# Kernel tuning notes

Measured on AMD Instinct MI355X. Metric: run time of the kernel, lower is better.

The kernel has to match this reference:

```python
import jax, jax.numpy as jnp
import numpy as np

NEG_BIG = 1e8  # diagonal mask penalty from the original code


def setup_inputs() -> dict:
    key = jax.random.key(0)
    ks = jax.random.split(key, 8)
    B, N, E, H, D, Hm = 2, 1024, 256, 64, 64, 128
    return {
        "encoder_output": jax.random.normal(ks[0], (B, N, E), dtype=jnp.float32),
        "wl": jax.random.normal(ks[1], (E, H), dtype=jnp.float32) * (1.0 / np.sqrt(E)),
        "wr": jax.random.normal(ks[2], (E, H), dtype=jnp.float32) * (1.0 / np.sqrt(E)),
        "u": jax.random.normal(ks[3], (H,), dtype=jnp.float32) * (1.0 / np.sqrt(H)),
        "l_bias": jnp.zeros((1,), dtype=jnp.float32),
        "edge_query": jax.random.normal(ks[4], (N, D), dtype=jnp.float32),
        "mlp_w1": jax.random.normal(ks[5], (D, Hm), dtype=jnp.float32) * (1.0 / np.sqrt(D)),
        "mlp_b1": jnp.zeros((Hm,), dtype=jnp.float32),
        "mlp_w2": jax.random.normal(ks[6], (Hm, 1), dtype=jnp.float32) * (1.0 / np.sqrt(Hm)),
        "mlp_b2": jnp.zeros((1,), dtype=jnp.float32),
    }


def reference(encoder_output, wl, wr, u, l_bias, edge_query, mlp_w1, mlp_b1, mlp_w2, mlp_b2):
    # edge-weight MLP: [E_edges, d] -> [E_edges]
    w_logits = (jax.nn.relu(edge_query @ mlp_w1 + mlp_b1) @ mlp_w2 + mlp_b2)[:, 0]
    w = jax.nn.softplus(w_logits) + 1e-8

    # pairwise additive attention logits
    dot_l = jnp.einsum("bne,eh->bnh", encoder_output, wl)  # [B,N,H]
    dot_r = jnp.einsum("bne,eh->bnh", encoder_output, wr)  # [B,N,H]
    final_sum = jnp.tanh(dot_l[:, :, None, :] + dot_r[:, None, :, :])  # [B,N,N,H]
    logits = jnp.einsum("bijh,h->bij", final_sum, u) + l_bias[0]  # [B,N,N]

    # vectorized diagonal masking (replaces the per-node python loop)
    N = logits.shape[1]
    eye = jnp.eye(N, dtype=logits.dtype)
    mask_scores = logits - NEG_BIG * eye[None, :, :]  # [B,N,N]

    probs = jax.nn.sigmoid(mask_scores)
    samples = (jax.random.uniform(jax.random.key(1), mask_scores.shape) < probs).astype(logits.dtype)
    # Bernoulli entropy from logits: softplus(l) - l * sigmoid(l)
    entropy = jax.nn.softplus(mask_scores) - mask_scores * probs
    return samples, mask_scores, entropy, w
```

## Files before the change

### kernel.cpp

```cpp
#include <hip/hip_runtime.h>
#include <hip/hip_bf16.h>


#define L2E 1.4426950408889634f
#define C2  2.8853900817779268f
#define LN2 0.6931471805599453f
#define RCP(x) __builtin_amdgcn_rcpf(x)
#define EXP2(x) __builtin_amdgcn_exp2f(x)
#define LOG2(x) __builtin_amdgcn_logf(x)

__device__ __forceinline__ void threefry2x32_01(unsigned x0, unsigned x1,
                                                unsigned& o0, unsigned& o1) {
  const unsigned k0 = 0u, k1 = 1u;
  const unsigned k2 = 0x1BD11BDAu ^ k0 ^ k1;
#define TF_R(r) { x0 += x1; x1 = (x1 << r) | (x1 >> (32 - r)); x1 ^= x0; }
  x0 += k0; x1 += k1;
  TF_R(13) TF_R(15) TF_R(26) TF_R(6)
  x0 += k1; x1 += k2 + 1u;
  TF_R(17) TF_R(29) TF_R(16) TF_R(24)
  x0 += k2; x1 += k0 + 2u;
  TF_R(13) TF_R(15) TF_R(26) TF_R(6)
  x0 += k0; x1 += k1 + 3u;
  TF_R(17) TF_R(29) TF_R(16) TF_R(24)
  x0 += k1; x1 += k2 + 4u;
  TF_R(13) TF_R(15) TF_R(26) TF_R(6)
  x0 += k2; x1 += k0 + 5u;
#undef TF_R
  o0 = x0; o1 = x1;
}

__device__ __forceinline__ float tf_uniform(unsigned y) {
  return __uint_as_float((y >> 9) | 0x3f800000u) - 1.0f;
}

__global__ __launch_bounds__(128) void edge_mlp_kernel(
    const float* __restrict__ eq, const float* __restrict__ w1,
    const float* __restrict__ b1, const float* __restrict__ w2,
    const float* __restrict__ b2, float* __restrict__ wout) {
  __shared__ float eql[64];
  __shared__ float part[2];
  const int t = threadIdx.x;
  const int e = blockIdx.x;
  if (t < 64) eql[t] = eq[e * 64 + t];
  __syncthreads();
  float acc = b1[t];
#pragma unroll 8
  for (int k = 0; k < 64; ++k) acc = fmaf(eql[k], w1[k * 128 + t], acc);
  float v = fmaxf(acc, 0.0f) * w2[t];
#pragma unroll
  for (int off = 32; off > 0; off >>= 1) v += __shfl_down(v, off);
  if ((t & 63) == 0) part[t >> 6] = v;
  __syncthreads();
  if (t == 0) {
    const float l = part[0] + part[1] + b2[0];
    const float sp = fmaxf(l, 0.0f) + log1pf(expf(-fabsf(l)));
    wout[e] = sp + 1e-8f;
  }
}

__global__ __launch_bounds__(256) void proj_exp_kernel(
    const float* __restrict__ enc, const float* __restrict__ wl,
    const float* __restrict__ wr, float* __restrict__ ws) {
  __shared__ float As[32][33];
  __shared__ float Ws[32][34];
  const int t = threadIdx.x;
  const int r0 = blockIdx.x * 32;
  const int c0 = blockIdx.y * 32;
  const float* __restrict__ wmat = (c0 < 64) ? wl : wr;
  const int cbase = c0 & 63;
  const int ty = t >> 4, tx = t & 15;
  float acc[2][2] = {};
  for (int ec = 0; ec < 8; ++ec) {
    {
      const int rr = t >> 3, e4 = (t & 7) * 4;
      const float4 v = *(const float4*)(enc + (r0 + rr) * 256 + ec * 32 + e4);
      As[rr][e4] = v.x; As[rr][e4 + 1] = v.y; As[rr][e4 + 2] = v.z; As[rr][e4 + 3] = v.w;
      const float4 w = *(const float4*)(wmat + (ec * 32 + rr) * 64 + cbase + e4);
      Ws[rr][e4] = w.x; Ws[rr][e4 + 1] = w.y; Ws[rr][e4 + 2] = w.z; Ws[rr][e4 + 3] = w.w;
    }
    __syncthreads();
#pragma unroll
    for (int e = 0; e < 32; ++e) {
      const float a0 = As[2 * ty][e];
      const float a1 = As[2 * ty + 1][e];
      const float2 wv = *(const float2*)&Ws[e][2 * tx];
      acc[0][0] = fmaf(a0, wv.x, acc[0][0]);
      acc[0][1] = fmaf(a0, wv.y, acc[0][1]);
      acc[1][0] = fmaf(a1, wv.x, acc[1][0]);
      acc[1][1] = fmaf(a1, wv.y, acc[1][1]);
    }
    __syncthreads();
  }
  const int matoff = (c0 < 64) ? 0 : 131072;
#pragma unroll
  for (int i = 0; i < 2; ++i) {
    const int r = r0 + 2 * ty + i;
    const int b = r >> 10, n = r & 1023;
#pragma unroll
    for (int j = 0; j < 2; ++j) {
      const int c = cbase + 2 * tx + j;
      ws[matoff + b * 65536 + c * 1024 + n] = EXP2(C2 * acc[i][j]);
    }
  }
}

__global__ __launch_bounds__(256) void pair_kernel(
    const float* __restrict__ ws, const float* __restrict__ u,
    const float* __restrict__ lb, float* __restrict__ out) {
  __shared__ float sA[2 * 64 * 64];
  __shared__ float sB[2 * 64 * 32];
  __shared__ float sU[64];
  const int t = threadIdx.x;
  const int i0 = blockIdx.x * 64;
  const int j0 = blockIdx.y * 32;

#pragma unroll
  for (int b = 0; b < 2; ++b) {
    const float* __restrict__ src = ws + b * 65536;
#pragma unroll
    for (int q = 0; q < 4; ++q) {
      const int h = (t >> 4) + 16 * q;
      const int c = (t & 15) * 4;
      *(float4*)(sA + b * 4096 + h * 64 + c) =
          *(const float4*)(src + h * 1024 + i0 + c);
    }
  }
#pragma unroll
  for (int b = 0; b < 2; ++b) {
    const float* __restrict__ src = ws + 131072 + b * 65536;
#pragma unroll
    for (int q = 0; q < 2; ++q) {
      const int h = (t >> 3) + 32 * q;
      const int c = (t & 7) * 4;
      *(float4*)(sB + b * 2048 + h * 32 + c) =
          *(const float4*)(src + h * 1024 + j0 + c);
    }
  }
  if (t < 64) sU[t] = u[t];
  __syncthreads();

  const int ia = (t >> 4) * 4;
  const int ja = (t & 15) * 2;
  float acc[2][4][2] = {};
#pragma unroll 4
  for (int h = 0; h < 64; ++h) {
    const float uh = sU[h];
#pragma unroll
    for (int b = 0; b < 2; ++b) {
      const float4 av = *(const float4*)(sA + b * 4096 + h * 64 + ia);
      const float2 bv = *(const float2*)(sB + b * 2048 + h * 32 + ja);
      const float a[4] = {av.x, av.y, av.z, av.w};
#pragma unroll
      for (int ii = 0; ii < 4; ++ii) {
        acc[b][ii][0] += uh * RCP(fmaf(a[ii], bv.x, 1.0f));
        acc[b][ii][1] += uh * RCP(fmaf(a[ii], bv.y, 1.0f));
      }
    }
  }

  float uv = sU[t & 63];
#pragma unroll
  for (int off = 32; off > 0; off >>= 1) uv += __shfl_xor(uv, off);
  const float su = uv + lb[0];

  float* __restrict__ outS = out;
  float* __restrict__ outM = out + 2097152;
  float* __restrict__ outE = out + 4194304;
#pragma unroll
  for (int ii = 0; ii < 4; ++ii) {
    const int gi = i0 + ia + ii;
    const unsigned mb = (unsigned)(gi * 1024 + j0 + ja);
    unsigned y00, y01, y10, y11;
    threefry2x32_01(mb, mb + 1048576u, y00, y01);
    threefry2x32_01(mb + 1u, mb + 1u + 1048576u, y10, y11);
    const float uu[2][2] = {{tf_uniform(y00), tf_uniform(y01)},
                            {tf_uniform(y10), tf_uniform(y11)}};
#pragma unroll
    for (int b = 0; b < 2; ++b) {
      float2 sv, ev, smv;
#pragma unroll
      for (int jj = 0; jj < 2; ++jj) {
        const int gj = j0 + ja + jj;
        float s = fmaf(-2.0f, acc[b][ii][jj], su);
        if (gi == gj) s -= 1e8f;
        const float ex = EXP2(-s * L2E);
        const float p = RCP(1.0f + ex);
        const float em = EXP2(-fabsf(s) * L2E);
        const float ent = fmaxf(s, 0.0f) + LOG2(1.0f + em) * LN2 - s * p;
        const float smp = (uu[jj][b] < p) ? 1.0f : 0.0f;
        (&sv.x)[jj] = s;
        (&ev.x)[jj] = ent;
        (&smv.x)[jj] = smp;
      }
      const int base = b * 1048576 + gi * 1024 + (j0 + ja);
      *(float2*)(outS + base) = smv;
      *(float2*)(outM + base) = sv;
      *(float2*)(outE + base) = ev;
    }
  }
}

extern "C" void kernel_launch(void* const* d_in, const int* in_sizes, int n_in,
                              void* d_out, int out_size, void* d_ws, size_t ws_size,
                              hipStream_t stream) {
  const float* enc = (const float*)d_in[0];
  const float* wl  = (const float*)d_in[1];
  const float* wr  = (const float*)d_in[2];
  const float* u   = (const float*)d_in[3];
  const float* lb  = (const float*)d_in[4];
  const float* eq  = (const float*)d_in[5];
  const float* w1  = (const float*)d_in[6];
  const float* b1  = (const float*)d_in[7];
  const float* w2  = (const float*)d_in[8];
  const float* b2  = (const float*)d_in[9];
  float* out = (float*)d_out;
  float* wsf = (float*)d_ws;

  edge_mlp_kernel<<<1024, 128, 0, stream>>>(eq, w1, b1, w2, b2, out + 6291456);
  proj_exp_kernel<<<dim3(64, 4), 256, 0, stream>>>(enc, wl, wr, wsf);
  pair_kernel<<<dim3(16, 32), 256, 0, stream>>>(wsf, u, lb, out);
}
```

Before: 112.3 us.

## Split pair kernel by batch and use square 4x4 register tiles

Moves the batch loop into the grid's z dimension and widens each block's j tile from 32 to 64, so every thread computes a 4x4 tile for a single batch. This gives a better ratio of shared-memory loads to reciprocal/FMA work and lets outputs go out as float4 stores. The threefry RNG is now computed twice per pair, once in each batch block, each keeping only one of its two outputs, which doubles RNG cost compared with sharing it across both batches.

```diff
diff --git a/kernel.cpp b/kernel.cpp
--- a/kernel.cpp
+++ b/kernel.cpp
@@ -107,55 +107,43 @@
 __global__ __launch_bounds__(256) void pair_kernel(
     const float* __restrict__ ws, const float* __restrict__ u,
     const float* __restrict__ lb, float* __restrict__ out) {
-  __shared__ float sA[2 * 64 * 64];
-  __shared__ float sB[2 * 64 * 32];
+  __shared__ float sA[64 * 64];
+  __shared__ float sB[64 * 64];
   __shared__ float sU[64];
   const int t = threadIdx.x;
+  const int b = blockIdx.z;
   const int i0 = blockIdx.x * 64;
-  const int j0 = blockIdx.y * 32;
-
-#pragma unroll
-  for (int b = 0; b < 2; ++b) {
-    const float* __restrict__ src = ws + b * 65536;
+  const int j0 = blockIdx.y * 64;
+  const float* __restrict__ srcA = ws + b * 65536;
+  const float* __restrict__ srcB = ws + 131072 + b * 65536;
+
+  {
+    const int lr = t >> 4, lc = (t & 15) * 4;
 #pragma unroll
     for (int q = 0; q < 4; ++q) {
-      const int h = (t >> 4) + 16 * q;
-      const int c = (t & 15) * 4;
-      *(float4*)(sA + b * 4096 + h * 64 + c) =
-          *(const float4*)(src + h * 1024 + i0 + c);
-    }
-  }
-#pragma unroll
-  for (int b = 0; b < 2; ++b) {
-    const float* __restrict__ src = ws + 131072 + b * 65536;
-#pragma unroll
-    for (int q = 0; q < 2; ++q) {
-      const int h = (t >> 3) + 32 * q;
-      const int c = (t & 7) * 4;
-      *(float4*)(sB + b * 2048 + h * 32 + c) =
-          *(const float4*)(src + h * 1024 + j0 + c);
+      const int h = lr + 16 * q;
+      *(float4*)(sA + h * 64 + lc) = *(const float4*)(srcA + h * 1024 + i0 + lc);
+      *(float4*)(sB + h * 64 + lc) = *(const float4*)(srcB + h * 1024 + j0 + lc);
     }
   }
   if (t < 64) sU[t] = u[t];
   __syncthreads();
 
   const int ia = (t >> 4) * 4;
-  const int ja = (t & 15) * 2;
-  float acc[2][4][2] = {};
+  const int ja = (t & 15) * 4;
+  float acc[4][4] = {};
 #pragma unroll 4
   for (int h = 0; h < 64; ++h) {
     const float uh = sU[h];
-#pragma unroll
-    for (int b = 0; b < 2; ++b) {
-      const float4 av = *(const float4*)(sA + b * 4096 + h * 64 + ia);
-      const float2 bv = *(const float2*)(sB + b * 2048 + h * 32 + ja);
-      const float a[4] = {av.x, av.y, av.z, av.w};
-#pragma unroll
-      for (int ii = 0; ii < 4; ++ii) {
-        acc[b][ii][0] += uh * RCP(fmaf(a[ii], bv.x, 1.0f));
-        acc[b][ii][1] += uh * RCP(fmaf(a[ii], bv.y, 1.0f));
-      }
-    }
+    const float4 av = *(const float4*)(sA + h * 64 + ia);
+    const float4 bv = *(const float4*)(sB + h * 64 + ja);
+    const float a[4] = {av.x, av.y, av.z, av.w};
+    const float bb[4] = {bv.x, bv.y, bv.z, bv.w};
+#pragma unroll
+    for (int ii = 0; ii < 4; ++ii)
+#pragma unroll
+      for (int jj = 0; jj < 4; ++jj)
+        acc[ii][jj] = fmaf(uh, RCP(fmaf(a[ii], bb[jj], 1.0f)), acc[ii][jj]);
   }
 
   float uv = sU[t & 63];
@@ -163,40 +151,34 @@
   for (int off = 32; off > 0; off >>= 1) uv += __shfl_xor(uv, off);
   const float su = uv + lb[0];
 
-  float* __restrict__ outS = out;
-  float* __restrict__ outM = out + 2097152;
-  float* __restrict__ outE = out + 4194304;
+  float* __restrict__ outS = out + b * 1048576;
+  float* __restrict__ outM = out + 2097152 + b * 1048576;
+  float* __restrict__ outE = out + 4194304 + b * 1048576;
 #pragma unroll
   for (int ii = 0; ii < 4; ++ii) {
     const int gi = i0 + ia + ii;
     const unsigned mb = (unsigned)(gi * 1024 + j0 + ja);
-    unsigned y00, y01, y10, y11;
-    threefry2x32_01(mb, mb + 1048576u, y00, y01);
-    threefry2x32_01(mb + 1u, mb + 1u + 1048576u, y10, y11);
-    const float uu[2][2] = {{tf_uniform(y00), tf_uniform(y01)},
-                            {tf_uniform(y10), tf_uniform(y11)}};
-#pragma unroll
-    for (int b = 0; b < 2; ++b) {
-      float2 sv, ev, smv;
-#pragma unroll
-      for (int jj = 0; jj < 2; ++jj) {
-        const int gj = j0 + ja + jj;
-        float s = fmaf(-2.0f, acc[b][ii][jj], su);
-        if (gi == gj) s -= 1e8f;
-        const float ex = EXP2(-s * L2E);
-        const float p = RCP(1.0f + ex);
-        const float em = EXP2(-fabsf(s) * L2E);
-        const float ent = fmaxf(s, 0.0f) + LOG2(1.0f + em) * LN2 - s * p;
-        const float smp = (uu[jj][b] < p) ? 1.0f : 0.0f;
-        (&sv.x)[jj] = s;
-        (&ev.x)[jj] = ent;
-        (&smv.x)[jj] = smp;
-      }
-      const int base = b * 1048576 + gi * 1024 + (j0 + ja);
-      *(float2*)(outS + base) = smv;
-      *(float2*)(outM + base) = sv;
-      *(float2*)(outE + base) = ev;
-    }
+    float4 sv, ev, smv;
+#pragma unroll
+    for (int jj = 0; jj < 4; ++jj) {
+      const int gj = j0 + ja + jj;
+      unsigned y0, y1;
+      threefry2x32_01(mb + (unsigned)jj, mb + (unsigned)jj + 1048576u, y0, y1);
+      const float uu = tf_uniform(b ? y1 : y0);
+      float s = fmaf(-2.0f, acc[ii][jj], su);
+      if (gi == gj) s -= 1e8f;
+      const float ex = EXP2(-s * L2E);
+      const float p = RCP(1.0f + ex);
+      const float em = EXP2(-fabsf(s) * L2E);
+      const float ent = fmaxf(s, 0.0f) + LOG2(1.0f + em) * LN2 - s * p;
+      (&sv.x)[jj] = s;
+      (&ev.x)[jj] = ent;
+      (&smv.x)[jj] = (uu < p) ? 1.0f : 0.0f;
+    }
+    const int base = gi * 1024 + j0 + ja;
+    *(float4*)(outS + base) = smv;
+    *(float4*)(outM + base) = sv;
+    *(float4*)(outE + base) = ev;
   }
 }
 
@@ -218,5 +200,5 @@
 
   edge_mlp_kernel<<<1024, 128, 0, stream>>>(eq, w1, b1, w2, b2, out + 6291456);
   proj_exp_kernel<<<dim3(64, 4), 256, 0, stream>>>(enc, wl, wr, wsf);
-  pair_kernel<<<dim3(16, 32), 256, 0, stream>>>(wsf, u, lb, out);
-}
+  pair_kernel<<<dim3(16, 16, 2), 256, 0, stream>>>(wsf, u, lb, out);
+}
```

Measured after the change: 112.6 us. About the same (+0.3%).
